# Performance work log

Measured on AMD Instinct MI355X. Metric: run time of the kernel, lower is better.

The kernel has to match this reference:

```python
import jax, jax.numpy as jnp
import numpy as np

B, N, M, D = 8, 1024, 2048, 1024


def setup_inputs() -> dict:
    key = jax.random.key(0)
    k1, k2, k3 = jax.random.split(key, 3)
    text_features = jax.random.normal(k1, (B, N, D), dtype=jnp.float32)
    audio_features = jax.random.normal(k2, (B, M, D), dtype=jnp.float32)
    sigma = jnp.ones((1,), dtype=jnp.float32)  # learnable bandwidth, initial_sigma=1.0
    # audio lengths in [M//4, M) so no softmax row is fully masked
    audio_lengths = jnp.maximum(
        jax.random.randint(k3, (B,), 0, M), M // 4
    ).astype(jnp.int32)
    return {
        "text_features": text_features,
        "audio_features": audio_features,
        "sigma": sigma,
        "audio_lengths": audio_lengths,
    }


def reference(text_features, audio_features, sigma, audio_lengths):
    b, n, d = text_features.shape
    m = audio_features.shape[1]
    s = jnp.abs(sigma[0]) + 1e-8

    # QK^T / sqrt(d)  -> (B, N, M)
    scores = jnp.einsum("bnd,bmd->bnm", text_features, audio_features) / jnp.sqrt(
        jnp.float32(d)
    )

    # Gaussian relative positional bias: -|i/N - j/M|^2 / (2 sigma^2)
    text_pos = jnp.arange(n, dtype=jnp.float32) / n    # (N,)
    audio_pos = jnp.arange(m, dtype=jnp.float32) / m   # (M,)
    d_rel = jnp.abs(text_pos[:, None] - audio_pos[None, :])  # (N, M)
    scores = scores - d_rel**2 / (2.0 * s * s)

    # mask padded audio positions per batch element
    valid = jnp.arange(m)[None, :] < audio_lengths[:, None]  # (B, M) bool
    scores = jnp.where(valid[:, None, :], scores, -jnp.inf)

    attention_weights = jax.nn.softmax(scores, axis=-1)  # (B, N, M)
    enhanced = jnp.einsum("bnm,bmd->bnd", attention_weights, audio_features)
    return enhanced, attention_weights
```

## Files before the change

kernel.cpp:

```cpp
#include <hip/hip_runtime.h>
#include <hip/hip_bf16.h>

#define BB 8
#define NN 1024
#define MM 2048
#define DD 1024

typedef __attribute__((ext_vector_type(8))) __bf16 bfrag8;
typedef __attribute__((ext_vector_type(4))) float ffrag4;

__device__ __forceinline__ unsigned short f2bf(float f) {
  union { float f; unsigned u; } x; x.f = f;
  unsigned r = x.u + 0x7FFFu + ((x.u >> 16) & 1u);
  return (unsigned short)(r >> 16);
}

__device__ __forceinline__ void gload_lds16(const unsigned short* g, unsigned short* l) {
  __builtin_amdgcn_global_load_lds(
      (const __attribute__((address_space(1))) void*)g,
      (__attribute__((address_space(3))) void*)l, 16, 0, 0);
}

#define SCHED0() __builtin_amdgcn_sched_barrier(0)
#define P_PRE()  do { SCHED0(); __builtin_amdgcn_s_barrier();                 \
                      asm volatile("s_waitcnt lgkmcnt(0)" ::: "memory");      \
                      SCHED0(); __builtin_amdgcn_s_setprio(1); } while (0)
#define P_POST() do { __builtin_amdgcn_s_setprio(0); SCHED0();                \
                      __builtin_amdgcn_s_barrier(); } while (0)

#define MFMA16x16x32 __builtin_amdgcn_mfma_f32_16x16x32_bf16

__device__ __forceinline__ void stage_half(const unsigned short* gbase, int ldk,
                                           unsigned short* ldst,
                                           int w, int r0, int slog) {
  const unsigned short* g = gbase + (size_t)(w * 8 + r0) * ldk + slog;
  gload_lds16(g, ldst + w * 512);
  gload_lds16(g + (size_t)64 * ldk, ldst + 4096 + w * 512);
}


__global__ __launch_bounds__(256) void ta_cvtQ(const float* __restrict__ Q,
                                               unsigned short* __restrict__ Qbf) {
  int t = blockIdx.x * 256 + threadIdx.x;
  const float4* src = reinterpret_cast<const float4*>(Q) + t * 2;
  float4 a = src[0], b = src[1];
  ushort4 lo = { f2bf(a.x), f2bf(a.y), f2bf(a.z), f2bf(a.w) };
  ushort4 hi = { f2bf(b.x), f2bf(b.y), f2bf(b.z), f2bf(b.w) };
  ushort4* dst = reinterpret_cast<ushort4*>(Qbf) + t * 2;
  dst[0] = lo; dst[1] = hi;
}

#define TSTR 68
__global__ __launch_bounds__(256) void ta_trans(const float* __restrict__ V,
                                                unsigned short* __restrict__ Kbf,
                                                unsigned short* __restrict__ VT) {
  const int dt = blockIdx.x;
  const int mt = blockIdx.y;
  const int b  = blockIdx.z;
  const int t  = threadIdx.x;
  __shared__ unsigned short Tls[64 * TSTR];

  const float* Vb = V + (size_t)b * MM * DD + (size_t)(mt * 64) * DD + dt * 64;
#pragma unroll
  for (int it = 0; it < 4; ++it) {
    int slot = t + 256 * it;
    int row  = slot >> 4;
    int c4   = slot & 15;
    float4 a = *reinterpret_cast<const float4*>(Vb + (size_t)row * DD + c4 * 4);
    ushort4 h = { f2bf(a.x), f2bf(a.y), f2bf(a.z), f2bf(a.w) };
    *reinterpret_cast<ushort4*>(&Tls[row * TSTR + c4 * 4]) = h;
  }
  __syncthreads();

  unsigned short* Kb = Kbf + (size_t)b * MM * DD + (size_t)(mt * 64) * DD + dt * 64;
  unsigned short* Vt = VT  + (size_t)b * DD * MM + (size_t)(dt * 64) * MM + mt * 64;
#pragma unroll
  for (int it = 0; it < 4; ++it) {
    int slot = t + 256 * it;
    int row  = slot >> 4;
    int c4   = slot & 15;
    *reinterpret_cast<ushort4*>(Kb + (size_t)row * DD + c4 * 4) =
        *reinterpret_cast<const ushort4*>(&Tls[row * TSTR + c4 * 4]);
    ushort4 tv = { Tls[(c4 * 4 + 0) * TSTR + row],
                   Tls[(c4 * 4 + 1) * TSTR + row],
                   Tls[(c4 * 4 + 2) * TSTR + row],
                   Tls[(c4 * 4 + 3) * TSTR + row] };
    *reinterpret_cast<ushort4*>(Vt + (size_t)row * MM + c4 * 4) = tv;
  }
}

__global__ void ta_zero(float* __restrict__ sums) {
  int t = blockIdx.x * 256 + threadIdx.x;
  if (t < BB * NN) sums[t] = 0.0f;
}

__global__ __launch_bounds__(512, 2) void ta_gemm1x(
    const unsigned short* __restrict__ Q,
    const unsigned short* __restrict__ K,
    const float* __restrict__ sigma,
    const int* __restrict__ lens,
    unsigned short* __restrict__ Ebf,
    float* __restrict__ rowsum)
{
  const int bj = blockIdx.x, bi = blockIdx.y, b = blockIdx.z;
  const int t = threadIdx.x;
  const int lane = t & 63, w = t >> 6;
  const int wr = w >> 2, wc = w & 3;
  __shared__ unsigned short S[65536];

  const unsigned short* Qb = Q + (size_t)b * NN * DD + (size_t)(bi * 256) * DD;
  const unsigned short* Kb = K + (size_t)b * MM * DD + (size_t)(bj * 256) * DD;

  const int r  = lane & 15, qd = lane >> 4;
  const int r0 = (lane >> 3) & 7;
  const int slog = ((lane & 7) ^ r0) << 3;
  const int cs0 = ((qd)     ^ (r & 7)) << 3;
  const int cs1 = ((4 + qd) ^ (r & 7)) << 3;

  ffrag4 acc[8][4] = {};

  {
    unsigned short* T0 = &S[0];
    stage_half(Qb,                        DD, T0,          w, r0, slog);
    stage_half(Qb + (size_t)128 * DD,     DD, T0 + 8192,   w, r0, slog);
    stage_half(Kb,                        DD, T0 + 16384,  w, r0, slog);
    stage_half(Kb + (size_t)128 * DD,     DD, T0 + 24576,  w, r0, slog);
    unsigned short* T1 = &S[32768];
    stage_half(Qb + 64,                    DD, T1,          w, r0, slog);
    stage_half(Qb + (size_t)128 * DD + 64, DD, T1 + 8192,   w, r0, slog);
    stage_half(Kb + 64,                    DD, T1 + 16384,  w, r0, slog);
    stage_half(Kb + (size_t)128 * DD + 64, DD, T1 + 24576,  w, r0, slog);
    asm volatile("s_waitcnt vmcnt(8)" ::: "memory");
    __builtin_amdgcn_s_barrier();
  }

  for (int kt = 0; kt < 16; ++kt) {
    const int p = kt & 1;
    unsigned short* Ab = &S[p * 32768 + wr * 8192];
    unsigned short* Bb = &S[p * 32768 + 16384 + (wc >> 1) * 8192];
    const int brb = (wc & 1) * 64;
    bfrag8 af[4][2], bf0[2][2], bf1[2][2];

#pragma unroll
    for (int mi = 0; mi < 4; ++mi) {
      const unsigned short* a = &Ab[(mi * 16 + r) * 64];
      af[mi][0] = *reinterpret_cast<const bfrag8*>(a + cs0);
      af[mi][1] = *reinterpret_cast<const bfrag8*>(a + cs1);
    }
#pragma unroll
    for (int jj = 0; jj < 2; ++jj) {
      const unsigned short* bp = &Bb[(brb + jj * 16 + r) * 64];
      bf0[jj][0] = *reinterpret_cast<const bfrag8*>(bp + cs0);
      bf0[jj][1] = *reinterpret_cast<const bfrag8*>(bp + cs1);
    }
    P_PRE();
#pragma unroll
    for (int mi = 0; mi < 4; ++mi)
#pragma unroll
      for (int jj = 0; jj < 2; ++jj) {
        acc[mi][jj] = MFMA16x16x32(af[mi][0], bf0[jj][0], acc[mi][jj], 0, 0, 0);
        acc[mi][jj] = MFMA16x16x32(af[mi][1], bf0[jj][1], acc[mi][jj], 0, 0, 0);
      }
    P_POST();

#pragma unroll
    for (int jj = 0; jj < 2; ++jj) {
      const unsigned short* bp = &Bb[(brb + (2 + jj) * 16 + r) * 64];
      bf1[jj][0] = *reinterpret_cast<const bfrag8*>(bp + cs0);
      bf1[jj][1] = *reinterpret_cast<const bfrag8*>(bp + cs1);
    }
    P_PRE();
#pragma unroll
    for (int mi = 0; mi < 4; ++mi)
#pragma unroll
      for (int jj = 0; jj < 2; ++jj) {
        acc[mi][2 + jj] = MFMA16x16x32(af[mi][0], bf1[jj][0], acc[mi][2 + jj], 0, 0, 0);
        acc[mi][2 + jj] = MFMA16x16x32(af[mi][1], bf1[jj][1], acc[mi][2 + jj], 0, 0, 0);
      }
    P_POST();

#pragma unroll
    for (int mi = 0; mi < 4; ++mi) {
      const unsigned short* a = &Ab[((mi + 4) * 16 + r) * 64];
      af[mi][0] = *reinterpret_cast<const bfrag8*>(a + cs0);
      af[mi][1] = *reinterpret_cast<const bfrag8*>(a + cs1);
    }
    if (kt + 2 < 16) {
      unsigned short* Dst = &S[p * 32768 + 16384];
      stage_half(Kb + (kt + 2) * 64,                    DD, Dst,        w, r0, slog);
      stage_half(Kb + (size_t)128 * DD + (kt + 2) * 64, DD, Dst + 8192, w, r0, slog);
    }
    P_PRE();
#pragma unroll
    for (int mi = 0; mi < 4; ++mi)
#pragma unroll
      for (int jj = 0; jj < 2; ++jj) {
        acc[4 + mi][2 + jj] = MFMA16x16x32(af[mi][0], bf1[jj][0], acc[4 + mi][2 + jj], 0, 0, 0);
        acc[4 + mi][2 + jj] = MFMA16x16x32(af[mi][1], bf1[jj][1], acc[4 + mi][2 + jj], 0, 0, 0);
      }
    P_POST();

    if (kt + 2 < 16) {
      unsigned short* Dst = &S[p * 32768];
      stage_half(Qb + (kt + 2) * 64,                    DD, Dst,        w, r0, slog);
      stage_half(Qb + (size_t)128 * DD + (kt + 2) * 64, DD, Dst + 8192, w, r0, slog);
    }
    P_PRE();
#pragma unroll
    for (int mi = 0; mi < 4; ++mi)
#pragma unroll
      for (int jj = 0; jj < 2; ++jj) {
        acc[4 + mi][jj] = MFMA16x16x32(af[mi][0], bf0[jj][0], acc[4 + mi][jj], 0, 0, 0);
        acc[4 + mi][jj] = MFMA16x16x32(af[mi][1], bf0[jj][1], acc[4 + mi][jj], 0, 0, 0);
      }
    __builtin_amdgcn_s_setprio(0);
    SCHED0();
    if (kt + 2 < 16)      { asm volatile("s_waitcnt vmcnt(8)" ::: "memory"); }
    else if (kt + 1 < 16) { asm volatile("s_waitcnt vmcnt(0)" ::: "memory"); }
    __builtin_amdgcn_s_barrier();
  }

  const float sg = fabsf(sigma[0]) + 1e-8f;
  const float inv2s2 = 1.0f / (2.0f * sg * sg);
  const int len = lens[b];
  unsigned short* Erow = Ebf + (size_t)b * NN * MM;
  float* sums = rowsum + (size_t)b * NN;
  const int ibase = bi * 256 + wr * 128;
  const int jbase = bj * 256 + wc * 64;
#pragma unroll
  for (int mi = 0; mi < 8; ++mi) {
#pragma unroll
    for (int v = 0; v < 4; ++v) {
      int i = ibase + mi * 16 + qd * 4 + v;
      float psum = 0.0f;
#pragma unroll
      for (int nj = 0; nj < 4; ++nj) {
        int j = jbase + nj * 16 + r;
        float e = 0.0f;
        if (j < len) {
          float dr = (float)i * (1.0f / (float)NN) - (float)j * (1.0f / (float)MM);
          float sc = acc[mi][nj][v] * 0.03125f - dr * dr * inv2s2;
          e = __expf(fminf(sc, 30.0f));
        }
        psum += e;
        Erow[(size_t)i * MM + j] = f2bf(e);
      }
      psum += __shfl_xor(psum, 1);
      psum += __shfl_xor(psum, 2);
      psum += __shfl_xor(psum, 4);
      psum += __shfl_xor(psum, 8);
      if (r == 0) atomicAdd(&sums[i], psum);
    }
  }
}

__global__ __launch_bounds__(512, 2) void ta_gemm2x(
    const unsigned short* __restrict__ E,
    const unsigned short* __restrict__ VT,
    const float* __restrict__ rowsum,
    float* __restrict__ O)
{
  const int bd = blockIdx.x, bi = blockIdx.y, b = blockIdx.z;
  const int t = threadIdx.x;
  const int lane = t & 63, w = t >> 6;
  const int wr = w >> 2, wc = w & 3;
  __shared__ unsigned short S[49152];

  const unsigned short* Eb = E  + (size_t)b * NN * MM + (size_t)(bi * 128) * MM;
  const unsigned short* Vb = VT + (size_t)b * DD * MM + (size_t)(bd * 256) * MM;

  const int r  = lane & 15, qd = lane >> 4;
  const int r0 = (lane >> 3) & 7;
  const int slog = ((lane & 7) ^ r0) << 3;
  const int cs0 = ((qd)     ^ (r & 7)) << 3;
  const int cs1 = ((4 + qd) ^ (r & 7)) << 3;

  ffrag4 acc[4][4] = {};

  {
    stage_half(Eb,                        MM, &S[0],     w, r0, slog);
    stage_half(Vb,                        MM, &S[8192],  w, r0, slog);
    stage_half(Vb + (size_t)128 * MM,     MM, &S[16384], w, r0, slog);
    stage_half(Eb + 64,                    MM, &S[24576],         w, r0, slog);
    stage_half(Vb + 64,                    MM, &S[24576 + 8192],  w, r0, slog);
    stage_half(Vb + (size_t)128 * MM + 64, MM, &S[24576 + 16384], w, r0, slog);
    asm volatile("s_waitcnt vmcnt(6)" ::: "memory");
    __builtin_amdgcn_s_barrier();
  }

  for (int kt = 0; kt < 32; ++kt) {
    const int p = kt & 1;
    unsigned short* Ab = &S[p * 24576];
    unsigned short* Bb = &S[p * 24576 + 8192 + (wc >> 1) * 8192];
    const int arb = wr * 64;
    const int brb = (wc & 1) * 64;
    bfrag8 af[2][2], bf0[2][2], bf1[2][2];

#pragma unroll
    for (int mi = 0; mi < 2; ++mi) {
      const unsigned short* a = &Ab[(arb + mi * 16 + r) * 64];
      af[mi][0] = *reinterpret_cast<const bfrag8*>(a + cs0);
      af[mi][1] = *reinterpret_cast<const bfrag8*>(a + cs1);
    }
#pragma unroll
    for (int jj = 0; jj < 2; ++jj) {
      const unsigned short* bp = &Bb[(brb + jj * 16 + r) * 64];
      bf0[jj][0] = *reinterpret_cast<const bfrag8*>(bp + cs0);
      bf0[jj][1] = *reinterpret_cast<const bfrag8*>(bp + cs1);
    }
    P_PRE();
#pragma unroll
    for (int mi = 0; mi < 2; ++mi)
#pragma unroll
      for (int jj = 0; jj < 2; ++jj) {
        acc[mi][jj] = MFMA16x16x32(af[mi][0], bf0[jj][0], acc[mi][jj], 0, 0, 0);
        acc[mi][jj] = MFMA16x16x32(af[mi][1], bf0[jj][1], acc[mi][jj], 0, 0, 0);
      }
    P_POST();

#pragma unroll
    for (int jj = 0; jj < 2; ++jj) {
      const unsigned short* bp = &Bb[(brb + (2 + jj) * 16 + r) * 64];
      bf1[jj][0] = *reinterpret_cast<const bfrag8*>(bp + cs0);
      bf1[jj][1] = *reinterpret_cast<const bfrag8*>(bp + cs1);
    }
    P_PRE();
#pragma unroll
    for (int mi = 0; mi < 2; ++mi)
#pragma unroll
      for (int jj = 0; jj < 2; ++jj) {
        acc[mi][2 + jj] = MFMA16x16x32(af[mi][0], bf1[jj][0], acc[mi][2 + jj], 0, 0, 0);
        acc[mi][2 + jj] = MFMA16x16x32(af[mi][1], bf1[jj][1], acc[mi][2 + jj], 0, 0, 0);
      }
    P_POST();

#pragma unroll
    for (int mi = 0; mi < 2; ++mi) {
      const unsigned short* a = &Ab[(arb + (mi + 2) * 16 + r) * 64];
      af[mi][0] = *reinterpret_cast<const bfrag8*>(a + cs0);
      af[mi][1] = *reinterpret_cast<const bfrag8*>(a + cs1);
    }
    if (kt + 2 < 32) {
      unsigned short* Dst = &S[p * 24576 + 8192];
      stage_half(Vb + (kt + 2) * 64,                    MM, Dst,        w, r0, slog);
      stage_half(Vb + (size_t)128 * MM + (kt + 2) * 64, MM, Dst + 8192, w, r0, slog);
    }
    P_PRE();
#pragma unroll
    for (int mi = 0; mi < 2; ++mi)
#pragma unroll
      for (int jj = 0; jj < 2; ++jj) {
        acc[2 + mi][2 + jj] = MFMA16x16x32(af[mi][0], bf1[jj][0], acc[2 + mi][2 + jj], 0, 0, 0);
        acc[2 + mi][2 + jj] = MFMA16x16x32(af[mi][1], bf1[jj][1], acc[2 + mi][2 + jj], 0, 0, 0);
      }
    P_POST();

    if (kt + 2 < 32) {
      stage_half(Eb + (kt + 2) * 64, MM, &S[p * 24576], w, r0, slog);
    }
    P_PRE();
#pragma unroll
    for (int mi = 0; mi < 2; ++mi)
#pragma unroll
      for (int jj = 0; jj < 2; ++jj) {
        acc[2 + mi][jj] = MFMA16x16x32(af[mi][0], bf0[jj][0], acc[2 + mi][jj], 0, 0, 0);
        acc[2 + mi][jj] = MFMA16x16x32(af[mi][1], bf0[jj][1], acc[2 + mi][jj], 0, 0, 0);
      }
    __builtin_amdgcn_s_setprio(0);
    SCHED0();
    if (kt + 2 < 32)      { asm volatile("s_waitcnt vmcnt(6)" ::: "memory"); }
    else if (kt + 1 < 32) { asm volatile("s_waitcnt vmcnt(0)" ::: "memory"); }
    __builtin_amdgcn_s_barrier();
  }

  float* Ob = O + (size_t)b * NN * DD;
  const float* rs = rowsum + (size_t)b * NN;
  const int ibase = bi * 128 + wr * 64;
  const int dbase = bd * 256 + wc * 64;
#pragma unroll
  for (int mi = 0; mi < 4; ++mi) {
#pragma unroll
    for (int v = 0; v < 4; ++v) {
      int i = ibase + mi * 16 + qd * 4 + v;
      float inv = 1.0f / fmaxf(rs[i], 1e-30f);
#pragma unroll
      for (int nj = 0; nj < 4; ++nj) {
        int d = dbase + nj * 16 + r;
        Ob[(size_t)i * DD + d] = acc[mi][nj][v] * inv;
      }
    }
  }
}

__global__ __launch_bounds__(256) void ta_normA(
    const unsigned short* __restrict__ Ebf,
    const float* __restrict__ sums,
    float* __restrict__ attn)
{
  int t = blockIdx.x * 256 + threadIdx.x;
  int row = t >> 8;
  const float inv = 1.0f / fmaxf(sums[row], 1e-30f);
  uint4 x = *(reinterpret_cast<const uint4*>(Ebf) + t);
  unsigned u[4] = { x.x, x.y, x.z, x.w };
  float o[8];
#pragma unroll
  for (int k = 0; k < 4; ++k) {
    union { unsigned u; float f; } lo, hi;
    lo.u = u[k] << 16; hi.u = u[k] & 0xFFFF0000u;
    o[2 * k]     = lo.f * inv;
    o[2 * k + 1] = hi.f * inv;
  }
  float4* dst = reinterpret_cast<float4*>(attn) + t * 2;
  float4 f0 = { o[0], o[1], o[2], o[3] };
  float4 f1 = { o[4], o[5], o[6], o[7] };
  dst[0] = f0; dst[1] = f1;
}

#define LDA 40
__global__ __launch_bounds__(256) void tb_gemm1e(
    const float* __restrict__ Q, const float* __restrict__ K,
    const float* __restrict__ sigma, const int* __restrict__ lens,
    float* __restrict__ attn, float* __restrict__ rowsum)
{
  const int bj = blockIdx.x, bi = blockIdx.y, b = blockIdx.z;
  const int t = threadIdx.x;
  const int lane = t & 63;
  const int w = t >> 6;
  const int wi = w >> 1, wj = w & 1;
  __shared__ unsigned short Als[128 * LDA];
  __shared__ unsigned short Bls[128 * LDA];
  const float* Qb = Q + (size_t)b * NN * DD + (size_t)(bi * 128) * DD;
  const float* Kb = K + (size_t)b * MM * DD + (size_t)(bj * 128) * DD;
  ffrag4 acc[4][4] = {};
  const int r = lane & 15;
  const int koff = (lane >> 4) * 8;
  for (int k0 = 0; k0 < DD; k0 += 32) {
#pragma unroll
    for (int it = 0; it < 4; ++it) {
      int slot = t + 256 * it;
      int row = slot >> 3, c4 = slot & 7;
      float4 qa = *reinterpret_cast<const float4*>(Qb + (size_t)row * DD + k0 + c4 * 4);
      float4 ka = *reinterpret_cast<const float4*>(Kb + (size_t)row * DD + k0 + c4 * 4);
      ushort4 qh = { f2bf(qa.x), f2bf(qa.y), f2bf(qa.z), f2bf(qa.w) };
      ushort4 kh = { f2bf(ka.x), f2bf(ka.y), f2bf(ka.z), f2bf(ka.w) };
      *reinterpret_cast<ushort4*>(&Als[row * LDA + c4 * 4]) = qh;
      *reinterpret_cast<ushort4*>(&Bls[row * LDA + c4 * 4]) = kh;
    }
    __syncthreads();
    bfrag8 af[4], bf[4];
#pragma unroll
    for (int ti = 0; ti < 4; ++ti)
      af[ti] = *reinterpret_cast<const bfrag8*>(&Als[(wi * 64 + ti * 16 + r) * LDA + koff]);
#pragma unroll
    for (int tj = 0; tj < 4; ++tj)
      bf[tj] = *reinterpret_cast<const bfrag8*>(&Bls[(wj * 64 + tj * 16 + r) * LDA + koff]);
#pragma unroll
    for (int ti = 0; ti < 4; ++ti)
#pragma unroll
      for (int tj = 0; tj < 4; ++tj)
        acc[ti][tj] = MFMA16x16x32(af[ti], bf[tj], acc[ti][tj], 0, 0, 0);
    __syncthreads();
  }
  const float s = fabsf(sigma[0]) + 1e-8f;
  const float inv2s2 = 1.0f / (2.0f * s * s);
  const int len = lens[b];
  float* Prow = attn + (size_t)b * NN * MM;
  float* sums = rowsum + (size_t)b * NN;
  const int ibase = bi * 128 + wi * 64;
  const int jbase = bj * 128 + wj * 64;
  const int quad = lane >> 4;
#pragma unroll
  for (int ti = 0; ti < 4; ++ti) {
#pragma unroll
    for (int v = 0; v < 4; ++v) {
      int i = ibase + ti * 16 + quad * 4 + v;
      float psum = 0.0f;
#pragma unroll
      for (int tj = 0; tj < 4; ++tj) {
        int j = jbase + tj * 16 + r;
        float e = 0.0f;
        if (j < len) {
          float dr = (float)i * (1.0f / (float)NN) - (float)j * (1.0f / (float)MM);
          float sc = acc[ti][tj][v] * 0.03125f - dr * dr * inv2s2;
          e = __expf(fminf(sc, 30.0f));
        }
        psum += e;
        Prow[(size_t)i * MM + j] = e;
      }
      psum += __shfl_xor(psum, 1);
      psum += __shfl_xor(psum, 2);
      psum += __shfl_xor(psum, 4);
      psum += __shfl_xor(psum, 8);
      if (r == 0) atomicAdd(&sums[i], psum);
    }
  }
}

__global__ __launch_bounds__(256) void tb_norm(float* __restrict__ attn,
                                               const float* __restrict__ sums) {
  int t = blockIdx.x * 256 + threadIdx.x;
  int row = t >> 9;
  const float inv = 1.0f / fmaxf(sums[row], 1e-30f);
  float4* p = reinterpret_cast<float4*>(attn) + t;
  float4 x = *p;
  x.x *= inv; x.y *= inv; x.z *= inv; x.w *= inv;
  *p = x;
}

__global__ __launch_bounds__(256) void tb_gemm2(
    const float* __restrict__ P, const float* __restrict__ V, float* __restrict__ O)
{
  const int bd = blockIdx.x, bi = blockIdx.y, b = blockIdx.z;
  const int t = threadIdx.x;
  const int lane = t & 63;
  const int w = t >> 6;
  const int wi = w >> 1, wj = w & 1;
  __shared__ unsigned short Pls[128 * LDA];
  __shared__ unsigned short Vls[128 * LDA];
  const float* Pb = P + (size_t)b * NN * MM + (size_t)(bi * 128) * MM;
  const float* Vb = V + (size_t)b * MM * DD + bd * 128;
  ffrag4 acc[4][4] = {};
  const int r = lane & 15;
  const int koff = (lane >> 4) * 8;
  const int vd = t & 127;
  const int vmb = (t >> 7) * 16;
  for (int k0 = 0; k0 < MM; k0 += 32) {
#pragma unroll
    for (int it = 0; it < 4; ++it) {
      int slot = t + 256 * it;
      int row = slot >> 3, c4 = slot & 7;
      float4 pa = *reinterpret_cast<const float4*>(Pb + (size_t)row * MM + k0 + c4 * 4);
      ushort4 ph = { f2bf(pa.x), f2bf(pa.y), f2bf(pa.z), f2bf(pa.w) };
      *reinterpret_cast<ushort4*>(&Pls[row * LDA + c4 * 4]) = ph;
    }
    union { unsigned short h[16]; uint4 q[2]; } hv;
#pragma unroll
    for (int i = 0; i < 16; ++i)
      hv.h[i] = f2bf(Vb[(size_t)(k0 + vmb + i) * DD + vd]);
    *reinterpret_cast<uint4*>(&Vls[vd * LDA + vmb]) = hv.q[0];
    *reinterpret_cast<uint4*>(&Vls[vd * LDA + vmb + 8]) = hv.q[1];
    __syncthreads();
    bfrag8 af[4], bf[4];
#pragma unroll
    for (int ti = 0; ti < 4; ++ti)
      af[ti] = *reinterpret_cast<const bfrag8*>(&Pls[(wi * 64 + ti * 16 + r) * LDA + koff]);
#pragma unroll
    for (int tj = 0; tj < 4; ++tj)
      bf[tj] = *reinterpret_cast<const bfrag8*>(&Vls[(wj * 64 + tj * 16 + r) * LDA + koff]);
#pragma unroll
    for (int ti = 0; ti < 4; ++ti)
#pragma unroll
      for (int tj = 0; tj < 4; ++tj)
        acc[ti][tj] = MFMA16x16x32(af[ti], bf[tj], acc[ti][tj], 0, 0, 0);
    __syncthreads();
  }
  float* Ob = O + (size_t)b * NN * DD;
  const int ibase = bi * 128 + wi * 64;
  const int dbase = bd * 128 + wj * 64;
#pragma unroll
  for (int ti = 0; ti < 4; ++ti) {
#pragma unroll
    for (int tj = 0; tj < 4; ++tj) {
      int d = dbase + tj * 16 + r;
#pragma unroll
      for (int v = 0; v < 4; ++v) {
        int i = ibase + ti * 16 + (lane >> 4) * 4 + v;
        Ob[(size_t)i * DD + d] = acc[ti][tj][v];
      }
    }
  }
}

extern "C" void kernel_launch(void* const* d_in, const int* in_sizes, int n_in,
                              void* d_out, int out_size, void* d_ws, size_t ws_size,
                              hipStream_t stream) {
  const float* text  = (const float*)d_in[0];
  const float* audio = (const float*)d_in[1];
  const float* sigma = (const float*)d_in[2];
  const int*   lens  = (const int*)d_in[3];

  float* out = (float*)d_out;
  float* enhanced = out;
  float* attn = out + (size_t)BB * NN * DD;

  const size_t QBF  = (size_t)BB * NN * DD * 2;
  const size_t KBF  = (size_t)BB * MM * DD * 2;
  const size_t VTB  = (size_t)BB * DD * MM * 2;
  const size_t EBF  = (size_t)BB * NN * MM * 2;
  const size_t offQ = 65536;
  const size_t offK = offQ + QBF;
  const size_t offV = offK + KBF;
  const size_t offE = offV + VTB;
  const size_t need = offE + EBF;

  float* rowsum = (float*)d_ws;

  if (ws_size >= need) {
    unsigned short* Qbf = (unsigned short*)((char*)d_ws + offQ);
    unsigned short* Kbf = (unsigned short*)((char*)d_ws + offK);
    unsigned short* VT  = (unsigned short*)((char*)d_ws + offV);
    unsigned short* Ebf = (unsigned short*)((char*)d_ws + offE);

    ta_zero<<<dim3((BB * NN + 255) / 256), 256, 0, stream>>>(rowsum);
    ta_cvtQ<<<dim3(BB * NN * DD / 8 / 256), 256, 0, stream>>>(text, Qbf);
    ta_trans<<<dim3(DD / 64, MM / 64, BB), 256, 0, stream>>>(audio, Kbf, VT);
    ta_gemm1x<<<dim3(MM / 256, NN / 256, BB), 512, 0, stream>>>(Qbf, Kbf, sigma, lens, Ebf, rowsum);
    ta_normA<<<dim3(BB * NN * MM / 8 / 256), 256, 0, stream>>>(Ebf, rowsum, attn);
    ta_gemm2x<<<dim3(DD / 256, NN / 128, BB), 512, 0, stream>>>(Ebf, VT, rowsum, enhanced);
  } else {
    ta_zero<<<dim3((BB * NN + 255) / 256), 256, 0, stream>>>(rowsum);
    tb_gemm1e<<<dim3(MM / 128, NN / 128, BB), 256, 0, stream>>>(text, audio, sigma, lens, attn, rowsum);
    tb_norm<<<dim3(BB * NN * MM / 4 / 256), 256, 0, stream>>>(attn, rowsum);
    tb_gemm2<<<dim3(DD / 128, NN / 128, BB), 256, 0, stream>>>(attn, audio, enhanced);
  }
}
```

Before: 280.4 us.

## Merge prep kernels into one launch and fuse attention normalization into gemm2 epilogue

The zero, Q-convert and K/V-transpose kernels are merged into one block-indexed prep kernel, which removes two launches. The separate normalization pass that wrote the fp32 attention weights now runs in the gemm2 epilogue. Each gemm2 block re-reads its 128x512 slice of bf16 E and writes the normalized fp32 weights, so one kernel launch goes away and the E reads may hit cache. The cost is a longer tail on gemm2 and a gemm2 grid that is smaller and less parallel for this store-heavy work.

```diff
diff --git a/kernel.cpp b/kernel.cpp
--- a/kernel.cpp
+++ b/kernel.cpp
@@ -38,54 +38,61 @@
   gload_lds16(g + (size_t)64 * ldk, ldst + 4096 + w * 512);
 }
 
-
-__global__ __launch_bounds__(256) void ta_cvtQ(const float* __restrict__ Q,
-                                               unsigned short* __restrict__ Qbf) {
-  int t = blockIdx.x * 256 + threadIdx.x;
-  const float4* src = reinterpret_cast<const float4*>(Q) + t * 2;
-  float4 a = src[0], b = src[1];
-  ushort4 lo = { f2bf(a.x), f2bf(a.y), f2bf(a.z), f2bf(a.w) };
-  ushort4 hi = { f2bf(b.x), f2bf(b.y), f2bf(b.z), f2bf(b.w) };
-  ushort4* dst = reinterpret_cast<ushort4*>(Qbf) + t * 2;
-  dst[0] = lo; dst[1] = hi;
-}
-
 #define TSTR 68
-__global__ __launch_bounds__(256) void ta_trans(const float* __restrict__ V,
-                                                unsigned short* __restrict__ Kbf,
-                                                unsigned short* __restrict__ VT) {
-  const int dt = blockIdx.x;
-  const int mt = blockIdx.y;
-  const int b  = blockIdx.z;
-  const int t  = threadIdx.x;
+__global__ __launch_bounds__(256) void ta_prep(
+    const float* __restrict__ Q, const float* __restrict__ V,
+    unsigned short* __restrict__ Qbf,
+    unsigned short* __restrict__ Kbf, unsigned short* __restrict__ VT,
+    float* __restrict__ sums)
+{
   __shared__ unsigned short Tls[64 * TSTR];
-
-  const float* Vb = V + (size_t)b * MM * DD + (size_t)(mt * 64) * DD + dt * 64;
-#pragma unroll
-  for (int it = 0; it < 4; ++it) {
-    int slot = t + 256 * it;
-    int row  = slot >> 4;
-    int c4   = slot & 15;
-    float4 a = *reinterpret_cast<const float4*>(Vb + (size_t)row * DD + c4 * 4);
-    ushort4 h = { f2bf(a.x), f2bf(a.y), f2bf(a.z), f2bf(a.w) };
-    *reinterpret_cast<ushort4*>(&Tls[row * TSTR + c4 * 4]) = h;
-  }
-  __syncthreads();
-
-  unsigned short* Kb = Kbf + (size_t)b * MM * DD + (size_t)(mt * 64) * DD + dt * 64;
-  unsigned short* Vt = VT  + (size_t)b * DD * MM + (size_t)(dt * 64) * MM + mt * 64;
-#pragma unroll
-  for (int it = 0; it < 4; ++it) {
-    int slot = t + 256 * it;
-    int row  = slot >> 4;
-    int c4   = slot & 15;
-    *reinterpret_cast<ushort4*>(Kb + (size_t)row * DD + c4 * 4) =
-        *reinterpret_cast<const ushort4*>(&Tls[row * TSTR + c4 * 4]);
-    ushort4 tv = { Tls[(c4 * 4 + 0) * TSTR + row],
-                   Tls[(c4 * 4 + 1) * TSTR + row],
-                   Tls[(c4 * 4 + 2) * TSTR + row],
-                   Tls[(c4 * 4 + 3) * TSTR + row] };
-    *reinterpret_cast<ushort4*>(Vt + (size_t)row * MM + c4 * 4) = tv;
+  const int bid = blockIdx.x;
+  const int t = threadIdx.x;
+
+  if (bid < 4096) {
+    int tt = bid * 256 + t;
+    const float4* src = reinterpret_cast<const float4*>(Q) + tt * 2;
+    float4 a = src[0], b = src[1];
+    ushort4 lo = { f2bf(a.x), f2bf(a.y), f2bf(a.z), f2bf(a.w) };
+    ushort4 hi = { f2bf(b.x), f2bf(b.y), f2bf(b.z), f2bf(b.w) };
+    ushort4* dst = reinterpret_cast<ushort4*>(Qbf) + tt * 2;
+    dst[0] = lo; dst[1] = hi;
+  } else if (bid < 8192) {
+    const int id = bid - 4096;
+    const int dt = id & 15;
+    const int mt = (id >> 4) & 31;
+    const int b  = id >> 9;
+
+    const float* Vb = V + (size_t)b * MM * DD + (size_t)(mt * 64) * DD + dt * 64;
+#pragma unroll
+    for (int it = 0; it < 4; ++it) {
+      int slot = t + 256 * it;
+      int row  = slot >> 4;
+      int c4   = slot & 15;
+      float4 a = *reinterpret_cast<const float4*>(Vb + (size_t)row * DD + c4 * 4);
+      ushort4 h = { f2bf(a.x), f2bf(a.y), f2bf(a.z), f2bf(a.w) };
+      *reinterpret_cast<ushort4*>(&Tls[row * TSTR + c4 * 4]) = h;
+    }
+    __syncthreads();
+
+    unsigned short* Kb = Kbf + (size_t)b * MM * DD + (size_t)(mt * 64) * DD + dt * 64;
+    unsigned short* Vt = VT  + (size_t)b * DD * MM + (size_t)(dt * 64) * MM + mt * 64;
+#pragma unroll
+    for (int it = 0; it < 4; ++it) {
+      int slot = t + 256 * it;
+      int row  = slot >> 4;
+      int c4   = slot & 15;
+      *reinterpret_cast<ushort4*>(Kb + (size_t)row * DD + c4 * 4) =
+          *reinterpret_cast<const ushort4*>(&Tls[row * TSTR + c4 * 4]);
+      ushort4 tv = { Tls[(c4 * 4 + 0) * TSTR + row],
+                     Tls[(c4 * 4 + 1) * TSTR + row],
+                     Tls[(c4 * 4 + 2) * TSTR + row],
+                     Tls[(c4 * 4 + 3) * TSTR + row] };
+      *reinterpret_cast<ushort4*>(Vt + (size_t)row * MM + c4 * 4) = tv;
+    }
+  } else {
+    int tt = (bid - 8192) * 256 + t;
+    sums[tt] = 0.0f;
   }
 }
 
@@ -258,7 +265,8 @@
     const unsigned short* __restrict__ E,
     const unsigned short* __restrict__ VT,
     const float* __restrict__ rowsum,
-    float* __restrict__ O)
+    float* __restrict__ O,
+    float* __restrict__ attn)
 {
   const int bd = blockIdx.x, bi = blockIdx.y, b = blockIdx.z;
   const int t = threadIdx.x;
@@ -390,30 +398,32 @@
       }
     }
   }
-}
-
-__global__ __launch_bounds__(256) void ta_normA(
-    const unsigned short* __restrict__ Ebf,
-    const float* __restrict__ sums,
-    float* __restrict__ attn)
-{
-  int t = blockIdx.x * 256 + threadIdx.x;
-  int row = t >> 8;
-  const float inv = 1.0f / fmaxf(sums[row], 1e-30f);
-  uint4 x = *(reinterpret_cast<const uint4*>(Ebf) + t);
-  unsigned u[4] = { x.x, x.y, x.z, x.w };
-  float o[8];
-#pragma unroll
-  for (int k = 0; k < 4; ++k) {
-    union { unsigned u; float f; } lo, hi;
-    lo.u = u[k] << 16; hi.u = u[k] & 0xFFFF0000u;
-    o[2 * k]     = lo.f * inv;
-    o[2 * k + 1] = hi.f * inv;
-  }
-  float4* dst = reinterpret_cast<float4*>(attn) + t * 2;
-  float4 f0 = { o[0], o[1], o[2], o[3] };
-  float4 f1 = { o[4], o[5], o[6], o[7] };
-  dst[0] = f0; dst[1] = f1;
+
+  {
+    float* attnB = attn + ((size_t)b * NN + bi * 128) * MM + bd * 512;
+    const unsigned short* Eslice = Eb + bd * 512;
+#pragma unroll
+    for (int it = 0; it < 16; ++it) {
+      int c = t + it * 512;
+      int row = c >> 6;
+      int col = (c & 63) * 8;
+      float inv = 1.0f / fmaxf(rs[bi * 128 + row], 1e-30f);
+      uint4 x = *reinterpret_cast<const uint4*>(Eslice + (size_t)row * MM + col);
+      unsigned u[4] = { x.x, x.y, x.z, x.w };
+      float o[8];
+#pragma unroll
+      for (int k = 0; k < 4; ++k) {
+        union { unsigned u; float f; } lo, hi;
+        lo.u = u[k] << 16; hi.u = u[k] & 0xFFFF0000u;
+        o[2 * k]     = lo.f * inv;
+        o[2 * k + 1] = hi.f * inv;
+      }
+      float4* dst = reinterpret_cast<float4*>(attnB + (size_t)row * MM + col);
+      float4 f0 = { o[0], o[1], o[2], o[3] };
+      float4 f1 = { o[4], o[5], o[6], o[7] };
+      dst[0] = f0; dst[1] = f1;
+    }
+  }
 }
 
 #define LDA 40
@@ -601,12 +611,9 @@
     unsigned short* VT  = (unsigned short*)((char*)d_ws + offV);
     unsigned short* Ebf = (unsigned short*)((char*)d_ws + offE);
 
-    ta_zero<<<dim3((BB * NN + 255) / 256), 256, 0, stream>>>(rowsum);
-    ta_cvtQ<<<dim3(BB * NN * DD / 8 / 256), 256, 0, stream>>>(text, Qbf);
-    ta_trans<<<dim3(DD / 64, MM / 64, BB), 256, 0, stream>>>(audio, Kbf, VT);
+    ta_prep<<<dim3(8224), 256, 0, stream>>>(text, audio, Qbf, Kbf, VT, rowsum);
     ta_gemm1x<<<dim3(MM / 256, NN / 256, BB), 512, 0, stream>>>(Qbf, Kbf, sigma, lens, Ebf, rowsum);
-    ta_normA<<<dim3(BB * NN * MM / 8 / 256), 256, 0, stream>>>(Ebf, rowsum, attn);
-    ta_gemm2x<<<dim3(DD / 256, NN / 128, BB), 512, 0, stream>>>(Ebf, VT, rowsum, enhanced);
+    ta_gemm2x<<<dim3(DD / 256, NN / 128, BB), 512, 0, stream>>>(Ebf, VT, rowsum, enhanced, attn);
   } else {
     ta_zero<<<dim3((BB * NN + 255) / 256), 256, 0, stream>>>(rowsum);
     tb_gemm1e<<<dim3(MM / 128, NN / 128, BB), 256, 0, stream>>>(text, audio, sigma, lens, attn, rowsum);
```

After: 276.6 us. Within noise of the previous version (-1.3%).
